# Kernel tuning notes

Hardware: AMD Instinct MI355X
Metric: run time of the kernel (lower is better)

Reference implementation:

```python
import jax, jax.numpy as jnp
import numpy as np

D = 2048; HQ = 16; HKV = 4; HD = 128
E = 8; F = 2048; FS = 11008; TOPK = 2
B = 2; S = 1024
EPS = 1e-6
NEG = -1e9


def setup_inputs() -> dict:
    key = jax.random.key(0)
    ks = jax.random.split(key, 16)
    p = lambda k, shape: jax.random.normal(k, shape, jnp.float32) * 0.02
    # rotary tables (rotate-half convention): [S, HD]
    pos = jnp.arange(S, dtype=jnp.float32)[:, None]
    inv = 1.0 / (10000.0 ** (jnp.arange(0, HD, 2, dtype=jnp.float32) / HD))
    ang = pos * inv[None, :]
    cos = jnp.concatenate([jnp.cos(ang), jnp.cos(ang)], axis=-1)
    sin = jnp.concatenate([jnp.sin(ang), jnp.sin(ang)], axis=-1)
    return dict(
        x=jax.random.normal(ks[0], (B, S, D), jnp.float32),
        rope_cos=cos, rope_sin=sin,
        attn_norm_w=jnp.ones((D,), jnp.float32),
        ffn_norm_w=jnp.ones((D,), jnp.float32),
        wq=p(ks[1], (D, HQ * HD)), bq=jnp.zeros((HQ * HD,), jnp.float32),
        wk=p(ks[2], (D, HKV * HD)), bk=jnp.zeros((HKV * HD,), jnp.float32),
        wv=p(ks[3], (D, HKV * HD)), bv=jnp.zeros((HKV * HD,), jnp.float32),
        wo=p(ks[4], (HQ * HD, D)),
        router_w=p(ks[5], (D, E)),
        w_gate=p(ks[6], (E, D, F)), w_up=p(ks[7], (E, D, F)), w_down=p(ks[8], (E, F, D)),
        ws_gate=p(ks[9], (D, FS)), ws_up=p(ks[10], (D, FS)), ws_down=p(ks[11], (FS, D)),
    )


def rmsnorm(x, w):
    return x * jax.lax.rsqrt(jnp.mean(x * x, axis=-1, keepdims=True) + EPS) * w


def rotate_half(x):
    x1, x2 = jnp.split(x, 2, axis=-1)
    return jnp.concatenate([-x2, x1], axis=-1)


def reference(x, rope_cos, rope_sin, attn_norm_w, ffn_norm_w,
              wq, bq, wk, bk, wv, bv, wo, router_w,
              w_gate, w_up, w_down, ws_gate, ws_up, ws_down):
    b, s, d = x.shape
    # ---- attention sublayer ----
    h = rmsnorm(x, attn_norm_w)
    q = (h @ wq + bq).reshape(b, s, HQ, HD)
    k = (h @ wk + bk).reshape(b, s, HKV, HD)
    v = (h @ wv + bv).reshape(b, s, HKV, HD)
    cos = rope_cos[None, :, None, :]
    sin = rope_sin[None, :, None, :]
    q = q * cos + rotate_half(q) * sin
    k = k * cos + rotate_half(k) * sin
    rep = HQ // HKV
    k = jnp.repeat(k, rep, axis=2)   # [b,s,HQ,HD]
    v = jnp.repeat(v, rep, axis=2)
    scores = jnp.einsum('bqhd,bkhd->bhqk', q, k) / np.sqrt(HD).astype(np.float32)
    causal = jnp.tril(jnp.ones((s, s), bool))
    scores = jnp.where(causal[None, None], scores, NEG)
    attn = jax.nn.softmax(scores, axis=-1)
    o = jnp.einsum('bhqk,bkhd->bqhd', attn, v).reshape(b, s, HQ * HD) @ wo
    new_k, new_v = k, v
    x = x + o
    # ---- MoE sublayer ----
    hn = rmsnorm(x, ffn_norm_w).reshape(b * s, d)   # [T,D]
    logits = hn @ router_w                           # [T,E]
    probs = jax.nn.softmax(logits, axis=-1)
    topv, topi = jax.lax.top_k(probs, TOPK)          # [T,K]
    topv = topv / jnp.sum(topv, axis=-1, keepdims=True)
    onehot = jax.nn.one_hot(topi, E, dtype=hn.dtype)  # [T,K,E]
    wdense = jnp.einsum('tke,tk->te', onehot, topv)   # sparse combine weights [T,E]
    g = jnp.einsum('td,edf->tef', hn, w_gate)
    u = jnp.einsum('td,edf->tef', hn, w_up)
    y = jnp.einsum('tef,efd->ted', jax.nn.silu(g) * u, w_down)
    routed = jnp.einsum('ted,te->td', y, wdense)
    shared = (jax.nn.silu(hn @ ws_gate) * (hn @ ws_up)) @ ws_down
    moe = (routed + shared).reshape(b, s, d)
    # load-balancing aux loss (Switch/Mixtral convention)
    frac = jnp.mean(onehot, axis=(0, 1))             # fraction dispatched per expert
    pmean = jnp.mean(probs, axis=0)
    aux_loss = E * jnp.sum(frac * pmean)
    out = x + moe
    return out, (new_k, new_v), aux_loss
```

## Files before the change

kernel.cpp:

```cpp
#include <hip/hip_runtime.h>

typedef unsigned short u16;
typedef unsigned int u32;
typedef unsigned long long u64;
typedef __attribute__((ext_vector_type(4))) unsigned short u16x4;
typedef __attribute__((ext_vector_type(8))) unsigned short u16x8;
typedef __attribute__((ext_vector_type(4))) float f32x4;
typedef __attribute__((ext_vector_type(8))) __bf16 bf16x8;

#define DD 2048
#define TT 2048
#define FSH 11008

__device__ __forceinline__ float bf2f(u16 u) {
  union { u32 i; float f; } v; v.i = ((u32)u) << 16; return v.f;
}
__device__ __forceinline__ u16 f2bf(float f) {
  union { float f; u32 i; } v; v.f = f;
  u32 r = v.i + 0x7fffu + ((v.i >> 16) & 1u);
  return (u16)(r >> 16);
}
__device__ __forceinline__ void gld16(const void* g, void* l) {
  __builtin_amdgcn_global_load_lds((const __attribute__((address_space(1))) void*)g,
                                   (__attribute__((address_space(3))) void*)l, 16, 0, 0);
}

#define MFMA16(d, a, b) d = __builtin_amdgcn_mfma_f32_16x16x32_bf16(a, b, d, 0, 0, 0)

__global__ __launch_bounds__(256) void rmsnorm_k(const float* __restrict__ x,
                                                 const float* __restrict__ w,
                                                 u16* __restrict__ out) {
  const int t = threadIdx.x;
  const float* xr = x + (size_t)blockIdx.x * DD;
  float4 a = *(const float4*)(xr + t * 8);
  float4 b = *(const float4*)(xr + t * 8 + 4);
  float ss = a.x*a.x + a.y*a.y + a.z*a.z + a.w*a.w
           + b.x*b.x + b.y*b.y + b.z*b.z + b.w*b.w;
#pragma unroll
  for (int m = 1; m < 64; m <<= 1) ss += __shfl_xor(ss, m);
  __shared__ float red[4];
  if ((t & 63) == 0) red[t >> 6] = ss;
  __syncthreads();
  float sc = rsqrtf((red[0] + red[1] + red[2] + red[3]) * (1.f / DD) + 1e-6f);
  float4 wa = *(const float4*)(w + t * 8);
  float4 wb = *(const float4*)(w + t * 8 + 4);
  u16x8 o;
  o[0] = f2bf(a.x * sc * wa.x); o[1] = f2bf(a.y * sc * wa.y);
  o[2] = f2bf(a.z * sc * wa.z); o[3] = f2bf(a.w * sc * wa.w);
  o[4] = f2bf(b.x * sc * wb.x); o[5] = f2bf(b.y * sc * wb.y);
  o[6] = f2bf(b.z * sc * wb.z); o[7] = f2bf(b.w * sc * wb.w);
  *(u16x8*)(out + (size_t)blockIdx.x * DD + t * 8) = o;
}

__global__ __launch_bounds__(256) void transp_k(const float* __restrict__ W,
                                                u16* __restrict__ Wt, int R, int C) {
  __shared__ u16 tile[64 * 72];
  const size_t msz = (size_t)R * C;
  const float* Wm = W + msz * blockIdx.z;
  u16* Wtm = Wt + msz * blockIdx.z;
  const int t = threadIdx.x;
  const int n0 = blockIdx.x * 64, k0 = blockIdx.y * 64;
#pragma unroll
  for (int p = 0; p < 4; ++p) {
    const int kk = (t >> 4) + p * 16;
    const int nn = (t & 15) * 4;
    float4 v = *(const float4*)(Wm + (size_t)(k0 + kk) * C + n0 + nn);
    u16x4 o; o[0] = f2bf(v.x); o[1] = f2bf(v.y); o[2] = f2bf(v.z); o[3] = f2bf(v.w);
    *(u16x4*)(tile + kk * 72 + nn) = o;
  }
  __syncthreads();
#pragma unroll
  for (int p = 0; p < 2; ++p) {
    const int n = (t >> 3) + p * 32;
    const int kb = t & 7;
#pragma unroll
    for (int j = 0; j < 8; ++j) {
      const int k = kb + j * 8;
      Wtm[(size_t)(n0 + n) * R + k0 + k] = tile[k * 72 + n];
    }
  }
}

template <int EPI, bool EXPERT, bool INDIR, bool SPLITK>
__global__ __launch_bounds__(256) void gemm2(
    const u16* __restrict__ A, const u16* __restrict__ Bt, void* __restrict__ Cp,
    const void* __restrict__ aux, const float* __restrict__ slotw,
    const int* __restrict__ slot_tok, const int* __restrict__ tiletab,
    int M, int N, int K, int Kc) {
  __shared__ u16 lA[128 * 32];
  __shared__ u16 lB[128 * 32];
  const int t = threadIdx.x, w = t >> 6, l = t & 63;
  const int n0 = blockIdx.x * 128;
  int m0;
  if constexpr (EXPERT) {
    const int ntil = tiletab[0];
    if ((int)blockIdx.y >= ntil) return;
    const int e = tiletab[1 + blockIdx.y * 2];
    m0 = tiletab[2 + blockIdx.y * 2];
    Bt += (size_t)e * N * K;
  } else {
    m0 = blockIdx.y * 128;
  }
  int kbase = 0, KC = K;
  if constexpr (SPLITK) { kbase = blockIdx.z * Kc; KC = Kc; }
  const int srow = w * 16 + (l >> 2);
  const int scol = (l & 3) * 8;
  const int r0 = m0 + srow, r1 = m0 + srow + 64;
  const u16 *ag0, *ag1;
  if constexpr (INDIR) {
    ag0 = A + (size_t)slot_tok[r0] * K + scol + kbase;
    ag1 = A + (size_t)slot_tok[r1] * K + scol + kbase;
  } else {
    ag0 = A + (size_t)r0 * K + scol + kbase;
    ag1 = A + (size_t)r1 * K + scol + kbase;
  }
  const u16* bg0 = Bt + (size_t)(n0 + srow) * K + scol + kbase;
  const u16* bg1 = Bt + (size_t)(n0 + srow + 64) * K + scol + kbase;
  u16* la = lA + w * 512;
  u16* lb = lB + w * 512;
  const int l15 = l & 15, l4 = l >> 4;
  const int wm = w >> 1, wn = w & 1;
  const int fa = (wm * 64 + l15) * 32 + l4 * 8;
  const int fb = (wn * 64 + l15) * 32 + l4 * 8;
  f32x4 acc[4][4] = {};
  for (int ko = 0; ko < KC; ko += 32) {
    __syncthreads();
    gld16(ag0 + ko, la);
    gld16(ag1 + ko, la + 2048);
    gld16(bg0 + ko, lb);
    gld16(bg1 + ko, lb + 2048);
    asm volatile("s_waitcnt vmcnt(0)" ::: "memory");
    __syncthreads();
    bf16x8 af[4], bf[4];
#pragma unroll
    for (int i = 0; i < 4; ++i) {
      af[i] = *(const bf16x8*)(lA + fa + i * 512);
      bf[i] = *(const bf16x8*)(lB + fb + i * 512);
    }
#pragma unroll
    for (int mi = 0; mi < 4; ++mi)
#pragma unroll
      for (int ni = 0; ni < 4; ++ni)
        MFMA16(acc[mi][ni], af[mi], bf[ni]);
  }
  float* Cf = (float*)Cp;
  if constexpr (SPLITK) Cf += (size_t)blockIdx.z * M * N;
#pragma unroll
  for (int mi = 0; mi < 4; ++mi) {
#pragma unroll
    for (int r = 0; r < 4; ++r) {
      const int row = m0 + wm * 64 + mi * 16 + l4 * 4 + r;
#pragma unroll
      for (int ni = 0; ni < 4; ++ni) {
        const int col = n0 + wn * 64 + ni * 16 + l15;
        const size_t idx = (size_t)row * N + col;
        const float v = acc[mi][ni][r];
        if constexpr (EPI == 0) Cf[idx] = v;
        else if constexpr (EPI == 2) ((u16*)Cp)[idx] = f2bf(v);
        else if constexpr (EPI == 3) {
          const float g = bf2f(((const u16*)aux)[idx]);
          ((u16*)Cp)[idx] = f2bf(v * g / (1.f + __expf(-g)));
        } else {
          ((u16*)Cp)[idx] = f2bf(slotw[row] * v);
        }
      }
    }
  }
}

template <int EPI, bool SPLITK>
__global__ __launch_bounds__(512, 2) void gemm8(
    const u16* __restrict__ A, const u16* __restrict__ Bt, void* __restrict__ Cp,
    const u16* __restrict__ aux, int M, int N, int K) {
  __shared__ char lds[131072];
  const int t = threadIdx.x, w = t >> 6, l = t & 63;
  const int gx = gridDim.x;
  const int nwg = gx * gridDim.y;
  int wg = blockIdx.y * gx + blockIdx.x;
  wg = (wg & 7) * (nwg >> 3) + (wg >> 3);
  const int n0 = (wg % gx) * 256;
  const int m0 = (wg / gx) * 256;
  int kbase = 0, KC = K;
  if constexpr (SPLITK) {
    kbase = blockIdx.z * 2816;
    const int rem = K - kbase;
    KC = rem < 2816 ? rem : 2816;
  }
  const int ktiles = KC >> 6;
  const int wm = w >> 2, wn = w & 3;
  const int l15 = l & 15, l4 = l >> 4;
  const int sro = l >> 3, sc = l & 7;

  auto stage = [&](int b, int isB, int h, int kt) {
    if (kt >= ktiles) kt = ktiles - 1;
    const u16* src = isB ? Bt : A;
    const int row0 = isB ? n0 : m0;
    char* base = lds + b * 65536 + isB * 32768;
#pragma unroll
    for (int i = 0; i < 2; ++i) {
      const int q = i * 8 + w;
      const int r0 = isB ? (((q >> 2) << 6) + h * 32 + (q & 3) * 8)
                         : (((q & 8) << 4) + h * 64 + (q & 7) * 8);
      const int r = r0 + sro;
      const int cl = sc ^ (r & 7);
      gld16(src + (size_t)(row0 + r) * K + kbase + kt * 64 + cl * 8, base + r0 * 128);
    }
  };
  auto ldA = [&](int b, int mi, int ks) {
    const int row = wm * 128 + mi * 16 + l15;
    const int ch = (ks * 4 + l4) ^ (row & 7);
    return *(const bf16x8*)(lds + b * 65536 + row * 128 + ch * 16);
  };
  auto ldB = [&](int b, int ni, int ks) {
    const int row = wn * 64 + ni * 16 + l15;
    const int ch = (ks * 4 + l4) ^ (row & 7);
    return *(const bf16x8*)(lds + b * 65536 + 32768 + row * 128 + ch * 16);
  };

  f32x4 acc[8][4] = {};
  bf16x8 aR[4][2], b0[2][2], b1[2][2];

  stage(0, 0, 0, 0); stage(0, 1, 0, 0); stage(0, 1, 1, 0); stage(0, 0, 1, 0);
  stage(1, 0, 0, 1); stage(1, 1, 1, 1); stage(1, 0, 1, 1);
  asm volatile("s_waitcnt vmcnt(6)" ::: "memory");
  __builtin_amdgcn_s_barrier();

  for (int kt = 0; kt < ktiles; kt += 2) {
#pragma unroll
    for (int mi = 0; mi < 4; ++mi) { aR[mi][0] = ldA(0, mi, 0); aR[mi][1] = ldA(0, mi, 1); }
#pragma unroll
    for (int ni = 0; ni < 2; ++ni) { b0[ni][0] = ldB(0, ni, 0); b0[ni][1] = ldB(0, ni, 1); }
    stage(1, 1, 0, kt + 1);
    __builtin_amdgcn_s_barrier();
    asm volatile("s_waitcnt lgkmcnt(0)" ::: "memory");
    __builtin_amdgcn_s_setprio(1);
#pragma unroll
    for (int mi = 0; mi < 4; ++mi)
#pragma unroll
      for (int ni = 0; ni < 2; ++ni) {
        MFMA16(acc[mi][ni], aR[mi][0], b0[ni][0]);
        MFMA16(acc[mi][ni], aR[mi][1], b0[ni][1]);
      }
    __builtin_amdgcn_s_setprio(0);
    __builtin_amdgcn_s_barrier();
#pragma unroll
    for (int ni = 0; ni < 2; ++ni) { b1[ni][0] = ldB(0, ni + 2, 0); b1[ni][1] = ldB(0, ni + 2, 1); }
    stage(0, 0, 0, kt + 2);
    __builtin_amdgcn_s_barrier();
    asm volatile("s_waitcnt lgkmcnt(0)" ::: "memory");
    __builtin_amdgcn_s_setprio(1);
#pragma unroll
    for (int mi = 0; mi < 4; ++mi)
#pragma unroll
      for (int ni = 0; ni < 2; ++ni) {
        MFMA16(acc[mi][ni + 2], aR[mi][0], b1[ni][0]);
        MFMA16(acc[mi][ni + 2], aR[mi][1], b1[ni][1]);
      }
    __builtin_amdgcn_s_setprio(0);
    __builtin_amdgcn_s_barrier();
#pragma unroll
    for (int mi = 0; mi < 4; ++mi) { aR[mi][0] = ldA(0, mi + 4, 0); aR[mi][1] = ldA(0, mi + 4, 1); }
    stage(0, 1, 1, kt + 2);
    __builtin_amdgcn_s_barrier();
    asm volatile("s_waitcnt lgkmcnt(0)" ::: "memory");
    __builtin_amdgcn_s_setprio(1);
#pragma unroll
    for (int mi = 0; mi < 4; ++mi)
#pragma unroll
      for (int ni = 0; ni < 2; ++ni) {
        MFMA16(acc[mi + 4][ni + 2], aR[mi][0], b1[ni][0]);
        MFMA16(acc[mi + 4][ni + 2], aR[mi][1], b1[ni][1]);
      }
    __builtin_amdgcn_s_setprio(0);
    __builtin_amdgcn_s_barrier();
    stage(0, 0, 1, kt + 2);
    __builtin_amdgcn_s_barrier();
    __builtin_amdgcn_s_setprio(1);
#pragma unroll
    for (int mi = 0; mi < 4; ++mi)
#pragma unroll
      for (int ni = 0; ni < 2; ++ni) {
        MFMA16(acc[mi + 4][ni], aR[mi][0], b0[ni][0]);
        MFMA16(acc[mi + 4][ni], aR[mi][1], b0[ni][1]);
      }
    __builtin_amdgcn_s_setprio(0);
    asm volatile("s_waitcnt vmcnt(6)" ::: "memory");
    __builtin_amdgcn_s_barrier();
#pragma unroll
    for (int mi = 0; mi < 4; ++mi) { aR[mi][0] = ldA(1, mi, 0); aR[mi][1] = ldA(1, mi, 1); }
#pragma unroll
    for (int ni = 0; ni < 2; ++ni) { b0[ni][0] = ldB(1, ni, 0); b0[ni][1] = ldB(1, ni, 1); }
    stage(0, 1, 0, kt + 2);
    __builtin_amdgcn_s_barrier();
    asm volatile("s_waitcnt lgkmcnt(0)" ::: "memory");
    __builtin_amdgcn_s_setprio(1);
#pragma unroll
    for (int mi = 0; mi < 4; ++mi)
#pragma unroll
      for (int ni = 0; ni < 2; ++ni) {
        MFMA16(acc[mi][ni], aR[mi][0], b0[ni][0]);
        MFMA16(acc[mi][ni], aR[mi][1], b0[ni][1]);
      }
    __builtin_amdgcn_s_setprio(0);
    __builtin_amdgcn_s_barrier();
#pragma unroll
    for (int ni = 0; ni < 2; ++ni) { b1[ni][0] = ldB(1, ni + 2, 0); b1[ni][1] = ldB(1, ni + 2, 1); }
    stage(1, 0, 0, kt + 3);
    __builtin_amdgcn_s_barrier();
    asm volatile("s_waitcnt lgkmcnt(0)" ::: "memory");
    __builtin_amdgcn_s_setprio(1);
#pragma unroll
    for (int mi = 0; mi < 4; ++mi)
#pragma unroll
      for (int ni = 0; ni < 2; ++ni) {
        MFMA16(acc[mi][ni + 2], aR[mi][0], b1[ni][0]);
        MFMA16(acc[mi][ni + 2], aR[mi][1], b1[ni][1]);
      }
    __builtin_amdgcn_s_setprio(0);
    __builtin_amdgcn_s_barrier();
#pragma unroll
    for (int mi = 0; mi < 4; ++mi) { aR[mi][0] = ldA(1, mi + 4, 0); aR[mi][1] = ldA(1, mi + 4, 1); }
    stage(1, 1, 1, kt + 3);
    __builtin_amdgcn_s_barrier();
    asm volatile("s_waitcnt lgkmcnt(0)" ::: "memory");
    __builtin_amdgcn_s_setprio(1);
#pragma unroll
    for (int mi = 0; mi < 4; ++mi)
#pragma unroll
      for (int ni = 0; ni < 2; ++ni) {
        MFMA16(acc[mi + 4][ni + 2], aR[mi][0], b1[ni][0]);
        MFMA16(acc[mi + 4][ni + 2], aR[mi][1], b1[ni][1]);
      }
    __builtin_amdgcn_s_setprio(0);
    __builtin_amdgcn_s_barrier();
    stage(1, 0, 1, kt + 3);
    __builtin_amdgcn_s_barrier();
    __builtin_amdgcn_s_setprio(1);
#pragma unroll
    for (int mi = 0; mi < 4; ++mi)
#pragma unroll
      for (int ni = 0; ni < 2; ++ni) {
        MFMA16(acc[mi + 4][ni], aR[mi][0], b0[ni][0]);
        MFMA16(acc[mi + 4][ni], aR[mi][1], b0[ni][1]);
      }
    __builtin_amdgcn_s_setprio(0);
    asm volatile("s_waitcnt vmcnt(6)" ::: "memory");
    __builtin_amdgcn_s_barrier();
  }

  u16* C16 = (u16*)Cp;
  if constexpr (EPI == 10) C16 += (size_t)blockIdx.z * ((size_t)M * N);
#pragma unroll
  for (int mi = 0; mi < 8; ++mi)
#pragma unroll
    for (int rr = 0; rr < 4; ++rr) {
      const int row = m0 + wm * 128 + mi * 16 + l4 * 4 + rr;
#pragma unroll
      for (int ni = 0; ni < 4; ++ni) {
        const int col = n0 + wn * 64 + ni * 16 + l15;
        const size_t idx = (size_t)row * N + col;
        const float v = acc[mi][ni][rr];
        if constexpr (EPI == 3) {
          const float g = bf2f(aux[idx]);
          C16[idx] = f2bf(v * g / (1.f + __expf(-g)));
        } else {
          C16[idx] = f2bf(v);
        }
      }
    }
}

template <int NP, bool ADDB>
__global__ __launch_bounds__(256) void red_k(float* __restrict__ dst,
                                             const float* __restrict__ base,
                                             const float* __restrict__ parts,
                                             int mn4) {
  const int i = blockIdx.x * 256 + threadIdx.x;
  float4 s;
  if constexpr (ADDB) s = ((const float4*)base)[i];
  else { s.x = s.y = s.z = s.w = 0.f; }
#pragma unroll
  for (int p = 0; p < NP; ++p) {
    const float4 v = ((const float4*)parts)[(size_t)p * mn4 + i];
    s.x += v.x; s.y += v.y; s.z += v.z; s.w += v.w;
  }
  ((float4*)dst)[i] = s;
}

__global__ __launch_bounds__(256) void redbf_k(float* __restrict__ dst,
                                               const float* __restrict__ base,
                                               const u16* __restrict__ parts) {
  const int i = blockIdx.x * 256 + threadIdx.x;
  float s[8];
  const float* bp = base + (size_t)i * 8;
#pragma unroll
  for (int j = 0; j < 8; ++j) s[j] = bp[j];
#pragma unroll
  for (int p = 0; p < 4; ++p) {
    u16x8 v = ((const u16x8*)parts)[(size_t)p * 524288 + i];
#pragma unroll
    for (int j = 0; j < 8; ++j) s[j] += bf2f(v[j]);
  }
  float* dp = dst + (size_t)i * 8;
#pragma unroll
  for (int j = 0; j < 8; ++j) dp[j] = s[j];
}

__global__ __launch_bounds__(256) void rope_k(
    const float* __restrict__ qkv, const float* __restrict__ cosb, const float* __restrict__ sinb,
    const float* __restrict__ bq, const float* __restrict__ bk, const float* __restrict__ bv,
    u16* __restrict__ QR, u16* __restrict__ KR, u16* __restrict__ VB,
    float* __restrict__ NK, float* __restrict__ NV) {
  const int s = blockIdx.x, b = blockIdx.y, t = threadIdx.x;
  const size_t tok = (size_t)b * 1024 + s;
  const float* row = qkv + tok * 3072;
  const float* cr = cosb + s * 128;
  const float* sr = sinb + s * 128;
  for (int i = t; i < 1024; i += 256) {
    const int h = i >> 6, d = i & 63;
    const float v1 = row[h * 128 + d] + bq[h * 128 + d];
    const float v2 = row[h * 128 + d + 64] + bq[h * 128 + d + 64];
    const float o1 = v1 * cr[d] - v2 * sr[d];
    const float o2 = v2 * cr[d + 64] + v1 * sr[d + 64];
    const size_t qb = (((size_t)(b * 16 + h)) * 1024 + s) * 128;
    QR[qb + d] = f2bf(o1);
    QR[qb + d + 64] = f2bf(o2);
  }
  {
    const int h = t >> 6, d = t & 63;
    const float v1 = row[2048 + h * 128 + d] + bk[h * 128 + d];
    const float v2 = row[2048 + h * 128 + d + 64] + bk[h * 128 + d + 64];
    const float o1 = v1 * cr[d] - v2 * sr[d];
    const float o2 = v2 * cr[d + 64] + v1 * sr[d + 64];
    const size_t kb = (((size_t)(b * 4 + h)) * 1024 + s) * 128;
    KR[kb + d] = f2bf(o1);
    KR[kb + d + 64] = f2bf(o2);
    const size_t ob = tok * 2048;
#pragma unroll
    for (int rep = 0; rep < 4; ++rep) {
      NK[ob + (h * 4 + rep) * 128 + d] = o1;
      NK[ob + (h * 4 + rep) * 128 + d + 64] = o2;
    }
  }
  for (int i = t; i < 512; i += 256) {
    const int h = i >> 7, d = i & 127;
    const float v = row[2560 + i] + bv[i];
    VB[(((size_t)(b * 4 + h)) * 1024 + s) * 128 + d] = f2bf(v);
    const size_t ob = tok * 2048;
#pragma unroll
    for (int rep = 0; rep < 4; ++rep) NV[ob + (h * 4 + rep) * 128 + d] = v;
  }
}

__global__ __launch_bounds__(256) void attn_k(const u16* __restrict__ Q,
                                              const u16* __restrict__ Kc,
                                              const u16* __restrict__ Vc,
                                              u16* __restrict__ O) {
  const int qt = blockIdx.x, h = blockIdx.y, b = blockIdx.z;
  const int t = threadIdx.x, w = t >> 6, l = t & 63;
  const int kvh = h >> 2;
  __shared__ u16 Ks[64 * 128];
  __shared__ u16 Vt[128 * 66];
  __shared__ u16 Ps[4][16 * 68];
  const int l15 = l & 15, l4 = l >> 4;
  bf16x8 qf[4];
  {
    const u16* qb = Q + (((size_t)(b * 16 + h)) * 1024 + qt * 64 + w * 16 + l15) * 128 + l4 * 8;
#pragma unroll
    for (int c = 0; c < 4; ++c) qf[c] = *(const bf16x8*)(qb + c * 32);
  }
  float m_run[4] = {-1e30f, -1e30f, -1e30f, -1e30f};
  float l_run[4] = {0.f, 0.f, 0.f, 0.f};
  f32x4 accO[8] = {};
  const size_t kvbase = ((size_t)(b * 4 + kvh)) * 1024 * 128;
  const int ntiles = qt + 1;
  for (int kt = 0; kt < ntiles; ++kt) {
    __syncthreads();
    {
      const int key = t >> 2;
      const u16* kg = Kc + kvbase + (size_t)(kt * 64 + key) * 128;
      const u16* vg = Vc + kvbase + (size_t)(kt * 64 + key) * 128;
      const int sw = (key & 7) << 4;
#pragma unroll
      for (int p = 0; p < 4; ++p) {
        const int ch = (t & 3) * 4 + p;
        *(u16x8*)((char*)Ks + key * 256 + ((ch * 16) ^ sw)) = *(const u16x8*)(kg + ch * 8);
        const int d0 = ch * 8;
        u16x8 vv = *(const u16x8*)(vg + d0);
#pragma unroll
        for (int j = 0; j < 8; ++j) Vt[(d0 + j) * 66 + key] = vv[j];
      }
    }
    __syncthreads();
    f32x4 sf[4] = {};
#pragma unroll
    for (int nf = 0; nf < 4; ++nf) {
      const int keyl = nf * 16 + l15;
      const int sw = (keyl & 7) << 4;
      const char* kbase = (const char*)Ks + keyl * 256;
#pragma unroll
      for (int c = 0; c < 4; ++c) {
        bf16x8 kf = *(const bf16x8*)(kbase + ((c * 64 + l4 * 16) ^ sw));
        sf[nf] = __builtin_amdgcn_mfma_f32_16x16x32_bf16(qf[c], kf, sf[nf], 0, 0, 0);
      }
    }
    const int qg0 = qt * 64 + w * 16 + l4 * 4;
    float alpha[4];
#pragma unroll
    for (int r = 0; r < 4; ++r) {
      const int qg = qg0 + r;
      float tm = -1e30f;
#pragma unroll
      for (int nf = 0; nf < 4; ++nf) {
        const int kg = kt * 64 + nf * 16 + l15;
        float sv = sf[nf][r] * 0.088388347648318447f;
        sv = (kg <= qg) ? sv : -1e30f;
        sf[nf][r] = sv;
        tm = fmaxf(tm, sv);
      }
#pragma unroll
      for (int mm = 1; mm < 16; mm <<= 1) tm = fmaxf(tm, __shfl_xor(tm, mm));
      const float mn = fmaxf(m_run[r], tm);
      alpha[r] = __expf(m_run[r] - mn);
      m_run[r] = mn;
      float rs = 0.f;
#pragma unroll
      for (int nf = 0; nf < 4; ++nf) {
        const float p = __expf(sf[nf][r] - mn);
        sf[nf][r] = p;
        rs += p;
      }
#pragma unroll
      for (int mm = 1; mm < 16; mm <<= 1) rs += __shfl_xor(rs, mm);
      l_run[r] = l_run[r] * alpha[r] + rs;
    }
#pragma unroll
    for (int nf = 0; nf < 8; ++nf)
#pragma unroll
      for (int r = 0; r < 4; ++r) accO[nf][r] *= alpha[r];
#pragma unroll
    for (int nf = 0; nf < 4; ++nf)
#pragma unroll
      for (int r = 0; r < 4; ++r)
        Ps[w][(l4 * 4 + r) * 68 + nf * 16 + l15] = f2bf(sf[nf][r]);
    __syncthreads();
#pragma unroll
    for (int kc = 0; kc < 2; ++kc) {
      const u16* pb = &Ps[w][0] + l15 * 68 + kc * 32 + l4 * 8;
      union { u16x4 q[2]; bf16x8 v; } pu;
      pu.q[0] = *(const u16x4*)pb;
      pu.q[1] = *(const u16x4*)(pb + 4);
#pragma unroll
      for (int nf = 0; nf < 8; ++nf) {
        const int dd = nf * 16 + l15;
        const u16* vp = &Vt[0] + dd * 66 + kc * 32 + l4 * 8;
        union { u32 u[4]; bf16x8 v; } vu;
        vu.u[0] = *(const u32*)(vp);
        vu.u[1] = *(const u32*)(vp + 2);
        vu.u[2] = *(const u32*)(vp + 4);
        vu.u[3] = *(const u32*)(vp + 6);
        accO[nf] = __builtin_amdgcn_mfma_f32_16x16x32_bf16(pu.v, vu.v, accO[nf], 0, 0, 0);
      }
    }
  }
  const int qg0 = qt * 64 + w * 16 + l4 * 4;
#pragma unroll
  for (int nf = 0; nf < 8; ++nf) {
    const int dd = nf * 16 + l15;
#pragma unroll
    for (int r = 0; r < 4; ++r) {
      const float o = accO[nf][r] / l_run[r];
      O[((size_t)(b * 1024 + qg0 + r)) * 2048 + h * 128 + dd] = f2bf(o);
    }
  }
}

__global__ __launch_bounds__(256) void router_k(
    const float* __restrict__ x2, const float* __restrict__ wn, const float* __restrict__ rw,
    int* __restrict__ topi2, float* __restrict__ topw2,
    int* __restrict__ counts, u64* __restrict__ pmean) {
  const int t = threadIdx.x, w = t >> 6, l = t & 63;
  const int tok = blockIdx.x * 4 + w;
  __shared__ int lc[8];
  __shared__ u64 lp[8];
  if (t < 8) { lc[t] = 0; lp[t] = 0ull; }
  __syncthreads();
  const float* xr = x2 + (size_t)tok * DD;
  float ss = 0.f;
#pragma unroll
  for (int i = 0; i < 8; ++i) {
    float4 v = *(const float4*)(xr + l * 32 + i * 4);
    ss += v.x * v.x + v.y * v.y + v.z * v.z + v.w * v.w;
  }
#pragma unroll
  for (int m = 1; m < 64; m <<= 1) ss += __shfl_xor(ss, m);
  const float sc = rsqrtf(ss * (1.f / DD) + 1e-6f);
  float acc[8] = {};
  for (int i = 0; i < 32; ++i) {
    const int d = l * 32 + i;
    const float hv = xr[d] * sc * wn[d];
    float4 r0 = *(const float4*)(rw + d * 8);
    float4 r1 = *(const float4*)(rw + d * 8 + 4);
    acc[0] += hv * r0.x; acc[1] += hv * r0.y; acc[2] += hv * r0.z; acc[3] += hv * r0.w;
    acc[4] += hv * r1.x; acc[5] += hv * r1.y; acc[6] += hv * r1.z; acc[7] += hv * r1.w;
  }
#pragma unroll
  for (int m = 1; m < 64; m <<= 1)
#pragma unroll
    for (int e = 0; e < 8; ++e) acc[e] += __shfl_xor(acc[e], m);
  if (l == 0) {
    float mx = acc[0];
#pragma unroll
    for (int e = 1; e < 8; ++e) mx = fmaxf(mx, acc[e]);
    float p[8], sum = 0.f;
#pragma unroll
    for (int e = 0; e < 8; ++e) { p[e] = __expf(acc[e] - mx); sum += p[e]; }
    const float inv = 1.f / sum;
#pragma unroll
    for (int e = 0; e < 8; ++e) p[e] *= inv;
    int e0 = 0; float v0 = p[0];
#pragma unroll
    for (int e = 1; e < 8; ++e) if (p[e] > v0) { v0 = p[e]; e0 = e; }
    int e1 = (e0 == 0) ? 1 : 0; float v1 = p[e1];
#pragma unroll
    for (int e = 0; e < 8; ++e) if (e != e0 && p[e] > v1) { v1 = p[e]; e1 = e; }
    const float wsum = v0 + v1;
    topi2[tok * 2] = e0; topi2[tok * 2 + 1] = e1;
    topw2[tok * 2] = v0 / wsum; topw2[tok * 2 + 1] = v1 / wsum;
    atomicAdd(&lc[e0], 1); atomicAdd(&lc[e1], 1);
#pragma unroll
    for (int e = 0; e < 8; ++e) atomicAdd(&lp[e], (u64)((double)p[e] * 4294967296.0));
  }
  __syncthreads();
  if (t < 8) {
    if (lc[t]) atomicAdd(&counts[t], lc[t]);
    if (lp[t]) atomicAdd(&pmean[t], lp[t]);
  }
}

__global__ __launch_bounds__(256) void zero_k(int* __restrict__ counts, u64* __restrict__ pmean,
                                              int* __restrict__ slot_tok, float* __restrict__ slot_w) {
  const int i = blockIdx.x * 256 + threadIdx.x;
  if (i < 5120) { slot_tok[i] = 0; slot_w[i] = 0.f; }
  if (i < 8) { counts[i] = 0; pmean[i] = 0ull; }
}

__global__ void scan_k(const int* __restrict__ counts, int* __restrict__ cursors,
                       int* __restrict__ tiletab, const u64* __restrict__ pmean,
                       float* __restrict__ auxout) {
  if (threadIdx.x == 0) {
    int off = 0, nt = 0;
    double aux = 0.0;
    for (int e = 0; e < 8; ++e) {
      cursors[e] = off;
      const int c = counts[e];
      const int nte = (c + 127) >> 7;
      for (int i = 0; i < nte; ++i) {
        tiletab[1 + nt * 2] = e;
        tiletab[2 + nt * 2] = off + i * 128;
        ++nt;
      }
      off += nte * 128;
      const double pm = ((double)pmean[e] / 4294967296.0) / 2048.0;
      aux += ((double)c / 4096.0) * pm;
    }
    tiletab[0] = nt;
    *auxout = (float)(8.0 * aux);
  }
}

__global__ __launch_bounds__(256) void assign_k(const int* __restrict__ topi2,
                                                const float* __restrict__ topw2,
                                                int* __restrict__ cursors,
                                                int* __restrict__ slot_tok,
                                                float* __restrict__ slot_w,
                                                int* __restrict__ tok_slot) {
  const int tok = blockIdx.x * 256 + threadIdx.x;
#pragma unroll
  for (int j = 0; j < 2; ++j) {
    const int e = topi2[tok * 2 + j];
    const int s = atomicAdd(&cursors[e], 1);
    slot_tok[s] = tok;
    slot_w[s] = topw2[tok * 2 + j];
    tok_slot[tok * 2 + j] = s;
  }
}

__global__ __launch_bounds__(256) void final_k(float* __restrict__ out,
                                               const u16* __restrict__ routed,
                                               const int* __restrict__ tok_slot) {
  const int tok = blockIdx.x, t = threadIdx.x;
  const int s0 = tok_slot[tok * 2], s1 = tok_slot[tok * 2 + 1];
  u16x8 a = ((const u16x8*)(routed + (size_t)s0 * DD))[t];
  u16x8 b = ((const u16x8*)(routed + (size_t)s1 * DD))[t];
  float* o = out + (size_t)tok * DD + t * 8;
  float4 o0 = *(const float4*)o;
  float4 o1 = *(const float4*)(o + 4);
  o0.x += bf2f(a[0]) + bf2f(b[0]); o0.y += bf2f(a[1]) + bf2f(b[1]);
  o0.z += bf2f(a[2]) + bf2f(b[2]); o0.w += bf2f(a[3]) + bf2f(b[3]);
  o1.x += bf2f(a[4]) + bf2f(b[4]); o1.y += bf2f(a[5]) + bf2f(b[5]);
  o1.z += bf2f(a[6]) + bf2f(b[6]); o1.w += bf2f(a[7]) + bf2f(b[7]);
  *(float4*)o = o0;
  *(float4*)(o + 4) = o1;
}

extern "C" void kernel_launch(void* const* d_in, const int* in_sizes, int n_in,
                              void* d_out, int out_size, void* d_ws, size_t ws_size,
                              hipStream_t stream) {
  (void)in_sizes; (void)n_in; (void)out_size; (void)ws_size;
  const float* x    = (const float*)d_in[0];
  const float* rc   = (const float*)d_in[1];
  const float* rs   = (const float*)d_in[2];
  const float* anw  = (const float*)d_in[3];
  const float* fnw  = (const float*)d_in[4];
  const float* wq   = (const float*)d_in[5];
  const float* bq   = (const float*)d_in[6];
  const float* wk   = (const float*)d_in[7];
  const float* bk   = (const float*)d_in[8];
  const float* wv   = (const float*)d_in[9];
  const float* bv   = (const float*)d_in[10];
  const float* wo   = (const float*)d_in[11];
  const float* rw   = (const float*)d_in[12];
  const float* wg   = (const float*)d_in[13];
  const float* wu   = (const float*)d_in[14];
  const float* wd   = (const float*)d_in[15];
  const float* wsg  = (const float*)d_in[16];
  const float* wsu  = (const float*)d_in[17];
  const float* wsd  = (const float*)d_in[18];

  const size_t MB = (size_t)1 << 20;
  char* ws = (char*)d_ws;
  float* X2  = (float*)(ws + 0);
  u16*   HN  = (u16*)(ws + 16 * MB);
  char*  SM  = ws + 24 * MB;
  char*  AR  = ws + 25 * MB;

  int*   CNT   = (int*)(SM);
  u64*   PM    = (u64*)(SM + 64);
  int*   CURS  = (int*)(SM + 256);
  int*   TILT  = (int*)(SM + 512);
  int*   TOPI  = (int*)(SM + 4096);
  float* TOPW  = (float*)(SM + 40960);
  int*   STOK  = (int*)(SM + 73728);
  float* SW    = (float*)(SM + 98304);
  int*   TSLOT = (int*)(SM + 131072);

  u16*   H      = (u16*)(AR);
  u16*   WTQ    = (u16*)(AR + 8 * MB);
  float* PARTSQ = (float*)(AR + 20 * MB);
  float* QKVF   = (float*)(AR + 68 * MB);
  u16*   QR    = (u16*)(AR);
  u16*   KR    = (u16*)(AR + 8 * MB);
  u16*   VBb   = (u16*)(AR + 10 * MB);
  u16*   ATTNO = (u16*)(AR + 12 * MB);
  u16*   WTO    = (u16*)(AR + 20 * MB);
  float* PARTSW = (float*)(AR + 28 * MB);
  u16*   WTS    = (u16*)(AR);
  u16*   G      = (u16*)(AR + 44 * MB);
  u16*   PARTSD = (u16*)(AR + 88 * MB);
  u16*   WTE    = (u16*)(AR);
  u16*   GEXP   = (u16*)(AR + 64 * MB);
  u16*   ROUTED = (u16*)(AR + 84 * MB);

  float* out  = (float*)d_out;
  float* NK   = out + 4194304;
  float* NV   = out + 2 * 4194304;
  float* AUXO = out + 3 * 4194304;

  const dim3 b256(256);
  const dim3 b512(512);

  rmsnorm_k<<<TT, b256, 0, stream>>>(x, anw, H);
  transp_k<<<dim3(32, 32, 1), b256, 0, stream>>>(wq, WTQ, 2048, 2048);
  transp_k<<<dim3(8, 32, 1), b256, 0, stream>>>(wk, WTQ + (size_t)2048 * 2048, 2048, 512);
  transp_k<<<dim3(8, 32, 1), b256, 0, stream>>>(wv, WTQ + (size_t)2560 * 2048, 2048, 512);
  gemm2<0, false, false, true><<<dim3(24, 16, 2), b256, 0, stream>>>(
      H, WTQ, PARTSQ, nullptr, nullptr, nullptr, nullptr, TT, 3072, 2048, 1024);
  red_k<2, false><<<6144, b256, 0, stream>>>(QKVF, nullptr, PARTSQ, 1572864);
  rope_k<<<dim3(1024, 2), b256, 0, stream>>>(QKVF, rc, rs, bq, bk, bv, QR, KR, VBb, NK, NV);
  attn_k<<<dim3(16, 16, 2), b256, 0, stream>>>(QR, KR, VBb, ATTNO);
  transp_k<<<dim3(32, 32, 1), b256, 0, stream>>>(wo, WTO, 2048, 2048);
  gemm2<0, false, false, true><<<dim3(16, 16, 4), b256, 0, stream>>>(
      ATTNO, WTO, PARTSW, nullptr, nullptr, nullptr, nullptr, TT, 2048, 2048, 512);
  red_k<4, true><<<4096, b256, 0, stream>>>(X2, x, PARTSW, 1048576);
  rmsnorm_k<<<TT, b256, 0, stream>>>(X2, fnw, HN);
  zero_k<<<20, b256, 0, stream>>>(CNT, PM, STOK, SW);
  router_k<<<512, b256, 0, stream>>>(X2, fnw, rw, TOPI, TOPW, CNT, PM);
  scan_k<<<1, 64, 0, stream>>>(CNT, CURS, TILT, PM, AUXO);
  assign_k<<<8, b256, 0, stream>>>(TOPI, TOPW, CURS, STOK, SW, TSLOT);
  transp_k<<<dim3(172, 32, 1), b256, 0, stream>>>(wsg, WTS, 2048, FSH);
  gemm8<2, false><<<dim3(43, 8, 1), b512, 0, stream>>>(HN, WTS, G, nullptr, TT, FSH, 2048);
  transp_k<<<dim3(172, 32, 1), b256, 0, stream>>>(wsu, WTS, 2048, FSH);
  gemm8<3, false><<<dim3(43, 8, 1), b512, 0, stream>>>(HN, WTS, G, G, TT, FSH, 2048);
  transp_k<<<dim3(32, 172, 1), b256, 0, stream>>>(wsd, WTS, FSH, 2048);
  gemm8<10, true><<<dim3(8, 8, 4), b512, 0, stream>>>(G, WTS, PARTSD, nullptr, TT, 2048, FSH);
  redbf_k<<<2048, b256, 0, stream>>>(out, X2, PARTSD);
  transp_k<<<dim3(32, 32, 8), b256, 0, stream>>>(wg, WTE, 2048, 2048);
  gemm2<2, true, true, false><<<dim3(16, 40, 1), b256, 0, stream>>>(
      HN, WTE, GEXP, nullptr, nullptr, STOK, TILT, 5120, 2048, 2048, 0);
  transp_k<<<dim3(32, 32, 8), b256, 0, stream>>>(wu, WTE, 2048, 2048);
  gemm2<3, true, true, false><<<dim3(16, 40, 1), b256, 0, stream>>>(
      HN, WTE, GEXP, GEXP, nullptr, STOK, TILT, 5120, 2048, 2048, 0);
  transp_k<<<dim3(32, 32, 8), b256, 0, stream>>>(wd, WTE, 2048, 2048);
  gemm2<4, true, false, false><<<dim3(16, 40, 1), b256, 0, stream>>>(
      GEXP, WTE, ROUTED, nullptr, SW, STOK, TILT, 5120, 2048, 2048, 0);
  final_k<<<TT, b256, 0, stream>>>(out, ROUTED, TSLOT);
}
```

Before: 1.036 ms.

## Route QKV and output projections through gemm8, vectorize transpose stores, precompute load addresses

The QKV and Wo projections move from the 128-tile gemm2 kernel to the 256x256 pipelined gemm8 kernel. gemm8 gains a runtime split-K chunk size and an fp32 partial-output epilogue (EPI 11) so it can feed the existing reduction kernels. The transpose kernel now writes the tile transposed into LDS so each thread emits one 16-byte global store instead of eight scalar stores. gemm8 precomputes its per-thread global and LDS staging addresses once rather than recomputing them every k-tile. The larger tiles give fewer workgroups on the smaller projection GEMMs, which may reduce occupancy.

```diff
diff --git a/kernel.cpp b/kernel.cpp
--- a/kernel.cpp
+++ b/kernel.cpp
@@ -54,7 +54,7 @@
 
 __global__ __launch_bounds__(256) void transp_k(const float* __restrict__ W,
                                                 u16* __restrict__ Wt, int R, int C) {
-  __shared__ u16 tile[64 * 72];
+  __shared__ u16 tile[64 * 80];
   const size_t msz = (size_t)R * C;
   const float* Wm = W + msz * blockIdx.z;
   u16* Wtm = Wt + msz * blockIdx.z;
@@ -65,19 +65,18 @@
     const int kk = (t >> 4) + p * 16;
     const int nn = (t & 15) * 4;
     float4 v = *(const float4*)(Wm + (size_t)(k0 + kk) * C + n0 + nn);
-    u16x4 o; o[0] = f2bf(v.x); o[1] = f2bf(v.y); o[2] = f2bf(v.z); o[3] = f2bf(v.w);
-    *(u16x4*)(tile + kk * 72 + nn) = o;
+    tile[(nn + 0) * 80 + kk] = f2bf(v.x);
+    tile[(nn + 1) * 80 + kk] = f2bf(v.y);
+    tile[(nn + 2) * 80 + kk] = f2bf(v.z);
+    tile[(nn + 3) * 80 + kk] = f2bf(v.w);
   }
   __syncthreads();
 #pragma unroll
   for (int p = 0; p < 2; ++p) {
     const int n = (t >> 3) + p * 32;
-    const int kb = t & 7;
-#pragma unroll
-    for (int j = 0; j < 8; ++j) {
-      const int k = kb + j * 8;
-      Wtm[(size_t)(n0 + n) * R + k0 + k] = tile[k * 72 + n];
-    }
+    const int c = t & 7;
+    u16x8 v = *(const u16x8*)(tile + n * 80 + c * 8);
+    *(u16x8*)(Wtm + (size_t)(n0 + n) * R + k0 + c * 8) = v;
   }
 }
 
@@ -171,7 +170,7 @@
 template <int EPI, bool SPLITK>
 __global__ __launch_bounds__(512, 2) void gemm8(
     const u16* __restrict__ A, const u16* __restrict__ Bt, void* __restrict__ Cp,
-    const u16* __restrict__ aux, int M, int N, int K) {
+    const u16* __restrict__ aux, int M, int N, int K, int Kc) {
   __shared__ char lds[131072];
   const int t = threadIdx.x, w = t >> 6, l = t & 63;
   const int gx = gridDim.x;
@@ -182,29 +181,37 @@
   const int m0 = (wg / gx) * 256;
   int kbase = 0, KC = K;
   if constexpr (SPLITK) {
-    kbase = blockIdx.z * 2816;
+    kbase = blockIdx.z * Kc;
     const int rem = K - kbase;
-    KC = rem < 2816 ? rem : 2816;
+    KC = rem < Kc ? rem : Kc;
   }
   const int ktiles = KC >> 6;
   const int wm = w >> 2, wn = w & 3;
   const int l15 = l & 15, l4 = l >> 4;
   const int sro = l >> 3, sc = l & 7;
 
+  const u16* sgp[2][2][2];
+  u32 sdo[2][2][2];
+#pragma unroll
+  for (int isB = 0; isB < 2; ++isB)
+#pragma unroll
+    for (int h = 0; h < 2; ++h)
+#pragma unroll
+      for (int i = 0; i < 2; ++i) {
+        const int q = i * 8 + w;
+        const int r0 = isB ? (((q >> 2) << 6) + h * 32 + (q & 3) * 8)
+                           : (((q & 8) << 4) + h * 64 + (q & 7) * 8);
+        const int r = r0 + sro;
+        const int cl = sc ^ (r & 7);
+        const u16* base = isB ? (Bt + (size_t)(n0 + r) * K) : (A + (size_t)(m0 + r) * K);
+        sgp[isB][h][i] = base + kbase + cl * 8;
+        sdo[isB][h][i] = (u32)(isB * 32768 + r0 * 128);
+      }
   auto stage = [&](int b, int isB, int h, int kt) {
-    if (kt >= ktiles) kt = ktiles - 1;
-    const u16* src = isB ? Bt : A;
-    const int row0 = isB ? n0 : m0;
-    char* base = lds + b * 65536 + isB * 32768;
-#pragma unroll
-    for (int i = 0; i < 2; ++i) {
-      const int q = i * 8 + w;
-      const int r0 = isB ? (((q >> 2) << 6) + h * 32 + (q & 3) * 8)
-                         : (((q & 8) << 4) + h * 64 + (q & 7) * 8);
-      const int r = r0 + sro;
-      const int cl = sc ^ (r & 7);
-      gld16(src + (size_t)(row0 + r) * K + kbase + kt * 64 + cl * 8, base + r0 * 128);
-    }
+    const int kk = kt < ktiles ? kt : ktiles - 1;
+#pragma unroll
+    for (int i = 0; i < 2; ++i)
+      gld16(sgp[isB][h][i] + kk * 64, lds + b * 65536 + sdo[isB][h][i]);
   };
   auto ldA = [&](int b, int mi, int ks) {
     const int row = wm * 128 + mi * 16 + l15;
@@ -349,7 +356,9 @@
   }
 
   u16* C16 = (u16*)Cp;
+  float* Cf = (float*)Cp;
   if constexpr (EPI == 10) C16 += (size_t)blockIdx.z * ((size_t)M * N);
+  if constexpr (EPI == 11) Cf += (size_t)blockIdx.z * ((size_t)M * N);
 #pragma unroll
   for (int mi = 0; mi < 8; ++mi)
 #pragma unroll
@@ -360,7 +369,9 @@
         const int col = n0 + wn * 64 + ni * 16 + l15;
         const size_t idx = (size_t)row * N + col;
         const float v = acc[mi][ni][rr];
-        if constexpr (EPI == 3) {
+        if constexpr (EPI == 11) {
+          Cf[idx] = v;
+        } else if constexpr (EPI == 3) {
           const float g = bf2f(aux[idx]);
           C16[idx] = f2bf(v * g / (1.f + __expf(-g)));
         } else {
@@ -774,14 +785,12 @@
   transp_k<<<dim3(32, 32, 1), b256, 0, stream>>>(wq, WTQ, 2048, 2048);
   transp_k<<<dim3(8, 32, 1), b256, 0, stream>>>(wk, WTQ + (size_t)2048 * 2048, 2048, 512);
   transp_k<<<dim3(8, 32, 1), b256, 0, stream>>>(wv, WTQ + (size_t)2560 * 2048, 2048, 512);
-  gemm2<0, false, false, true><<<dim3(24, 16, 2), b256, 0, stream>>>(
-      H, WTQ, PARTSQ, nullptr, nullptr, nullptr, nullptr, TT, 3072, 2048, 1024);
+  gemm8<11, true><<<dim3(12, 8, 2), b512, 0, stream>>>(H, WTQ, PARTSQ, nullptr, TT, 3072, 2048, 1024);
   red_k<2, false><<<6144, b256, 0, stream>>>(QKVF, nullptr, PARTSQ, 1572864);
   rope_k<<<dim3(1024, 2), b256, 0, stream>>>(QKVF, rc, rs, bq, bk, bv, QR, KR, VBb, NK, NV);
   attn_k<<<dim3(16, 16, 2), b256, 0, stream>>>(QR, KR, VBb, ATTNO);
   transp_k<<<dim3(32, 32, 1), b256, 0, stream>>>(wo, WTO, 2048, 2048);
-  gemm2<0, false, false, true><<<dim3(16, 16, 4), b256, 0, stream>>>(
-      ATTNO, WTO, PARTSW, nullptr, nullptr, nullptr, nullptr, TT, 2048, 2048, 512);
+  gemm8<11, true><<<dim3(8, 8, 4), b512, 0, stream>>>(ATTNO, WTO, PARTSW, nullptr, TT, 2048, 2048, 512);
   red_k<4, true><<<4096, b256, 0, stream>>>(X2, x, PARTSW, 1048576);
   rmsnorm_k<<<TT, b256, 0, stream>>>(X2, fnw, HN);
   zero_k<<<20, b256, 0, stream>>>(CNT, PM, STOK, SW);
@@ -789,11 +798,11 @@
   scan_k<<<1, 64, 0, stream>>>(CNT, CURS, TILT, PM, AUXO);
   assign_k<<<8, b256, 0, stream>>>(TOPI, TOPW, CURS, STOK, SW, TSLOT);
   transp_k<<<dim3(172, 32, 1), b256, 0, stream>>>(wsg, WTS, 2048, FSH);
-  gemm8<2, false><<<dim3(43, 8, 1), b512, 0, stream>>>(HN, WTS, G, nullptr, TT, FSH, 2048);
+  gemm8<2, false><<<dim3(43, 8, 1), b512, 0, stream>>>(HN, WTS, G, nullptr, TT, FSH, 2048, 2048);
   transp_k<<<dim3(172, 32, 1), b256, 0, stream>>>(wsu, WTS, 2048, FSH);
-  gemm8<3, false><<<dim3(43, 8, 1), b512, 0, stream>>>(HN, WTS, G, G, TT, FSH, 2048);
+  gemm8<3, false><<<dim3(43, 8, 1), b512, 0, stream>>>(HN, WTS, G, G, TT, FSH, 2048, 2048);
   transp_k<<<dim3(32, 172, 1), b256, 0, stream>>>(wsd, WTS, FSH, 2048);
-  gemm8<10, true><<<dim3(8, 8, 4), b512, 0, stream>>>(G, WTS, PARTSD, nullptr, TT, 2048, FSH);
+  gemm8<10, true><<<dim3(8, 8, 4), b512, 0, stream>>>(G, WTS, PARTSD, nullptr, TT, 2048, FSH, 2816);
   redbf_k<<<2048, b256, 0, stream>>>(out, X2, PARTSD);
   transp_k<<<dim3(32, 32, 8), b256, 0, stream>>>(wg, WTE, 2048, 2048);
   gemm2<2, true, true, false><<<dim3(16, 40, 1), b256, 0, stream>>>(
```

New measurement: 990.9 us. 4.4% less time.
